# Kernel tuning notes

Hardware: AMD Instinct MI355X
Metric: run time of the kernel (lower is better)

Reference implementation:

```python
import jax, jax.numpy as jnp
import numpy as np
from jax import lax

B, T, C, DIN, DOUT = 32, 128, 64, 32, 32  # batch, output_channels(seq), input_channels, input_dim, output_dim


def _init_params(key):
    # Mirror torch init: xOps zeros with identity on min(dout,din) diag; hOps = eye.
    # Add small noise so gradients/behavior are non-degenerate.
    k1, k2 = jax.random.split(key)
    eye_x = jnp.zeros((DOUT, DIN), jnp.float32).at[jnp.arange(min(DOUT, DIN)), jnp.arange(min(DOUT, DIN))].set(1.0)
    xOps = jnp.broadcast_to(eye_x, (4, T, C, DOUT, DIN)) + 0.02 * jax.random.normal(k1, (4, T, C, DOUT, DIN), jnp.float32)
    hOps = jnp.broadcast_to(jnp.eye(DOUT, dtype=jnp.float32), (4, T, C, DOUT, DOUT)) + 0.02 * jax.random.normal(k2, (4, T, C, DOUT, DOUT), jnp.float32)
    return xOps, hOps


def setup_inputs() -> dict:
    key = jax.random.key(0)
    kx, kp = jax.random.split(key)
    x = jax.random.normal(kx, (B, T, C, DIN), jnp.float32)
    xOps, hOps = _init_params(kp)
    return {"x": x, "xOps": xOps, "hOps": hOps}


def reference(x, xOps, hOps):
    # x: [B,T,C,Din]; xOps: [4,T,C,Dout,Din]; hOps: [4,T,C,Dout,Dout]
    b, t, c, _ = x.shape
    dout = hOps.shape[-1]
    h0 = jnp.zeros((b, c, dout), x.dtype)
    c0 = jnp.zeros((b, c, dout), x.dtype)

    def step(carry, inp):
        h, cc = carry
        x_t, xop_t, hop_t = inp  # [B,C,Din], [4,C,Dout,Din], [4,C,Dout,Dout]
        # per-channel (grouped) gate pre-activations, 4 gates at once
        X = jnp.einsum('gcij,bcj->gbci', xop_t, x_t) + jnp.einsum('gcij,bcj->gbci', hop_t, h)
        i = jax.nn.sigmoid(X[0])
        f = jax.nn.sigmoid(X[1])
        g = jnp.tanh(X[2])
        o = jax.nn.sigmoid(X[3])
        c_new = f * cc + i * g
        h_new = o * jnp.tanh(c_new)
        return (h_new, c_new), None

    xs = (jnp.swapaxes(x, 0, 1), jnp.swapaxes(xOps, 0, 1), jnp.swapaxes(hOps, 0, 1))
    (h_fin, _), _ = lax.scan(step, (h0, c0), xs)
    return h_fin  # [B,C,Dout]
```

## Files before the change

### kernel.cpp

```cpp
#include <hip/hip_runtime.h>
#include <stdint.h>

#define T_STEPS 128
#define C_CH    64
#define D_IN    32
#define D_OUT   32

#define RS 72

using frag_ab = __attribute__((ext_vector_type(8))) short;
using frag_cd = __attribute__((ext_vector_type(4))) float;

__device__ __forceinline__ void lds_barrier() {
  asm volatile("s_waitcnt lgkmcnt(0)\n\ts_barrier" ::: "memory");
}

__device__ __forceinline__ uint32_t pack_hi16(uint32_t u0, uint32_t u1) {
  return __builtin_amdgcn_perm(u1, u0, 0x07060302u);
}

__device__ __forceinline__ float fast_sigmoid(float v) {
  return __builtin_amdgcn_rcpf(1.0f + __expf(-v));
}
__device__ __forceinline__ float fast_tanh(float v) {
  return fmaf(2.0f, __builtin_amdgcn_rcpf(1.0f + __expf(-2.0f * v)), -1.0f);
}

__global__ void __launch_bounds__(256)
lstm_kernel(const float* __restrict__ x, const float* __restrict__ xOps,
            const float* __restrict__ hOps, float* __restrict__ out) {
  __shared__ short Ahi[128 * RS];
  __shared__ short Alo[128 * RS];
  __shared__ short Bhi[16 * RS];
  __shared__ short Blo[16 * RS];
  __shared__ float exch[4 * 32 * 9];

  const int tid = threadIdx.x;
  const int c   = blockIdx.x & 63;
  const int q   = blockIdx.x >> 6;

  for (int idx = tid; idx < (16 * RS) / 2; idx += 256) {
    ((uint32_t*)Bhi)[idx] = 0u;
    ((uint32_t*)Blo)[idx] = 0u;
  }

  const float* wptr[8];
  int wlds[8];
#pragma unroll
  for (int it = 0; it < 8; ++it) {
    int f  = (it * 256 + tid) * 4;
    int fh = f & 4095;
    int g  = fh >> 10;
    int i  = (fh >> 5) & 31;
    int j  = fh & 31;
    const float* base = (f < 4096) ? xOps : hOps;
    wptr[it] = base + (size_t)g * (T_STEPS * C_CH * 1024) + (size_t)c * 1024 + i * 32 + j;
    int k = j + ((f < 4096) ? 0 : 32);
    wlds[it] = (g * 32 + i) * RS + k;
  }

  const float* xptr = x;
  int xlds = 0;
  if (tid < 128) {
    int bl = tid >> 4;
    int kp = (tid & 15) * 2;
    int bg = q * 8 + bl;
    xptr = x + (size_t)bg * (T_STEPS * C_CH * D_IN) + (size_t)c * D_IN + kp;
    xlds = bl * RS + kp;
  }

  const int wave   = tid >> 6;
  const int lane   = tid & 63;
  const int frag_n = lane & 15;
  const int quad   = lane >> 4;

  const int eb = tid >> 5;
  const int ei = tid & 31;

  float4 wv[8];
#pragma unroll
  for (int it = 0; it < 8; ++it) wv[it] = *(const float4*)wptr[it];
  float2 xv = make_float2(0.f, 0.f);
  if (tid < 128) xv = *(const float2*)xptr;

  lds_barrier();

  float c_state = 0.0f;

#pragma unroll 1
  for (int t = 0; t < T_STEPS; ++t) {
#pragma unroll
    for (int it = 0; it < 8; ++it) {
      float4 v = wv[it];
      uint32_t u0 = __float_as_uint(v.x), u1 = __float_as_uint(v.y);
      uint32_t u2 = __float_as_uint(v.z), u3 = __float_as_uint(v.w);
      float r0 = v.x - __uint_as_float(u0 & 0xFFFF0000u);
      float r1 = v.y - __uint_as_float(u1 & 0xFFFF0000u);
      float r2 = v.z - __uint_as_float(u2 & 0xFFFF0000u);
      float r3 = v.w - __uint_as_float(u3 & 0xFFFF0000u);
      int s = wlds[it];
      *(uint2*)&Ahi[s] = make_uint2(pack_hi16(u0, u1), pack_hi16(u2, u3));
      *(uint2*)&Alo[s] = make_uint2(pack_hi16(__float_as_uint(r0), __float_as_uint(r1)),
                                    pack_hi16(__float_as_uint(r2), __float_as_uint(r3)));
    }
    if (tid < 128) {
      uint32_t u0 = __float_as_uint(xv.x), u1 = __float_as_uint(xv.y);
      float r0 = xv.x - __uint_as_float(u0 & 0xFFFF0000u);
      float r1 = xv.y - __uint_as_float(u1 & 0xFFFF0000u);
      *(uint32_t*)&Bhi[xlds] = pack_hi16(u0, u1);
      *(uint32_t*)&Blo[xlds] = pack_hi16(__float_as_uint(r0), __float_as_uint(r1));
    }

    if (t + 1 < T_STEPS) {
#pragma unroll
      for (int it = 0; it < 8; ++it)
        wv[it] = *(const float4*)(wptr[it] + (size_t)(t + 1) * (C_CH * 1024));
      if (tid < 128) xv = *(const float2*)(xptr + (size_t)(t + 1) * (C_CH * D_IN));
    }

    lds_barrier();

    frag_cd acc0 = {0.f, 0.f, 0.f, 0.f};
    frag_cd acc1 = {0.f, 0.f, 0.f, 0.f};
#pragma unroll
    for (int kt = 0; kt < 2; ++kt) {
      const int kk = kt * 32 + quad * 8;
      frag_ab bh = *(const frag_ab*)&Bhi[frag_n * RS + kk];
      frag_ab bl = *(const frag_ab*)&Blo[frag_n * RS + kk];
      {
        int m = wave * 32 + frag_n;
        frag_ab ah = *(const frag_ab*)&Ahi[m * RS + kk];
        frag_ab al = *(const frag_ab*)&Alo[m * RS + kk];
        acc0 = __builtin_amdgcn_mfma_f32_16x16x32_bf16(ah, bh, acc0, 0, 0, 0);
        acc0 = __builtin_amdgcn_mfma_f32_16x16x32_bf16(ah, bl, acc0, 0, 0, 0);
        acc0 = __builtin_amdgcn_mfma_f32_16x16x32_bf16(al, bh, acc0, 0, 0, 0);
      }
      {
        int m = wave * 32 + 16 + frag_n;
        frag_ab ah = *(const frag_ab*)&Ahi[m * RS + kk];
        frag_ab al = *(const frag_ab*)&Alo[m * RS + kk];
        acc1 = __builtin_amdgcn_mfma_f32_16x16x32_bf16(ah, bh, acc1, 0, 0, 0);
        acc1 = __builtin_amdgcn_mfma_f32_16x16x32_bf16(ah, bl, acc1, 0, 0, 0);
        acc1 = __builtin_amdgcn_mfma_f32_16x16x32_bf16(al, bh, acc1, 0, 0, 0);
      }
    }

    if (frag_n < 8) {
#pragma unroll
      for (int r = 0; r < 4; ++r) {
        exch[(wave * 32 + quad * 4 + r) * 9 + frag_n]      = acc0[r];
        exch[(wave * 32 + 16 + quad * 4 + r) * 9 + frag_n] = acc1[r];
      }
    }

    lds_barrier();

    {
      float X0 = exch[(0 * 32 + ei) * 9 + eb];
      float X1 = exch[(1 * 32 + ei) * 9 + eb];
      float X2 = exch[(2 * 32 + ei) * 9 + eb];
      float X3 = exch[(3 * 32 + ei) * 9 + eb];
      float ig = fast_sigmoid(X0);
      float fg = fast_sigmoid(X1);
      float gg = fast_tanh(X2);
      float og = fast_sigmoid(X3);
      c_state = fg * c_state + ig * gg;
      float hval = og * fast_tanh(c_state);
      if (t == T_STEPS - 1) {
        out[((size_t)(q * 8 + eb) * C_CH + c) * D_OUT + ei] = hval;
      } else {
        uint32_t u  = __float_as_uint(hval);
        float    r  = hval - __uint_as_float(u & 0xFFFF0000u);
        uint32_t ru = __float_as_uint(r);
        uint32_t pu  = __shfl_xor(u, 1, 64);
        uint32_t pru = __shfl_xor(ru, 1, 64);
        if ((ei & 1) == 0) {
          *(uint32_t*)&Bhi[eb * RS + 32 + ei] = pack_hi16(u, pu);
          *(uint32_t*)&Blo[eb * RS + 32 + ei] = pack_hi16(ru, pru);
        }
      }
    }
  }
}

extern "C" void kernel_launch(void* const* d_in, const int* in_sizes, int n_in,
                              void* d_out, int out_size, void* d_ws, size_t ws_size,
                              hipStream_t stream) {
  const float* x    = (const float*)d_in[0];
  const float* xOps = (const float*)d_in[1];
  const float* hOps = (const float*)d_in[2];
  lstm_kernel<<<dim3(256), dim3(256), 0, stream>>>(x, xOps, hOps, (float*)d_out);
}
```

Measured before the change: 359.2 us.

## Stream weights via async global-to-LDS loads with double buffering and in-register gates

Weight tiles now go straight from global memory into double-buffered LDS through global_load_lds, and the bf16 hi/lo split is done in registers at MFMA operand load time rather than on a staging write. Rows are permuted so each lane's accumulator holds all four gates for one output element, which removes the exchange buffer and one barrier per step. The block grows to 512 threads (8 waves), each issuing a single MFMA chain, and the loop is unrolled by two. This trades more threads, XOR-swizzled LDS indexing and a vmcnt wait per step for a shorter serial critical path per timestep.

```diff
diff --git a/kernel.cpp b/kernel.cpp
--- a/kernel.cpp
+++ b/kernel.cpp
@@ -3,17 +3,10 @@
 
 #define T_STEPS 128
 #define C_CH    64
-#define D_IN    32
-#define D_OUT   32
-
-#define RS 72
 
 using frag_ab = __attribute__((ext_vector_type(8))) short;
 using frag_cd = __attribute__((ext_vector_type(4))) float;
-
-__device__ __forceinline__ void lds_barrier() {
-  asm volatile("s_waitcnt lgkmcnt(0)\n\ts_barrier" ::: "memory");
-}
+typedef __attribute__((ext_vector_type(4))) uint32_t u32x4;
 
 __device__ __forceinline__ uint32_t pack_hi16(uint32_t u0, uint32_t u1) {
   return __builtin_amdgcn_perm(u1, u0, 0x07060302u);
@@ -26,159 +19,161 @@
   return fmaf(2.0f, __builtin_amdgcn_rcpf(1.0f + __expf(-2.0f * v)), -1.0f);
 }
 
-__global__ void __launch_bounds__(256)
+__device__ __forceinline__ void async_load16(const float* g, void* l) {
+  __builtin_amdgcn_global_load_lds((const __attribute__((address_space(1))) void*)g,
+                                   (__attribute__((address_space(3))) void*)l, 16, 0, 0);
+}
+
+struct Frag2 { frag_ab hi, lo; };
+
+__device__ __forceinline__ Frag2 split8(float4 a, float4 b) {
+  uint32_t u0 = __float_as_uint(a.x), u1 = __float_as_uint(a.y);
+  uint32_t u2 = __float_as_uint(a.z), u3 = __float_as_uint(a.w);
+  uint32_t u4 = __float_as_uint(b.x), u5 = __float_as_uint(b.y);
+  uint32_t u6 = __float_as_uint(b.z), u7 = __float_as_uint(b.w);
+  uint32_t r0 = __float_as_uint(a.x - __uint_as_float(u0 & 0xFFFF0000u));
+  uint32_t r1 = __float_as_uint(a.y - __uint_as_float(u1 & 0xFFFF0000u));
+  uint32_t r2 = __float_as_uint(a.z - __uint_as_float(u2 & 0xFFFF0000u));
+  uint32_t r3 = __float_as_uint(a.w - __uint_as_float(u3 & 0xFFFF0000u));
+  uint32_t r4 = __float_as_uint(b.x - __uint_as_float(u4 & 0xFFFF0000u));
+  uint32_t r5 = __float_as_uint(b.y - __uint_as_float(u5 & 0xFFFF0000u));
+  uint32_t r6 = __float_as_uint(b.z - __uint_as_float(u6 & 0xFFFF0000u));
+  uint32_t r7 = __float_as_uint(b.w - __uint_as_float(u7 & 0xFFFF0000u));
+  union { u32x4 v; frag_ab f; } H, L;
+  H.v[0] = pack_hi16(u0, u1); H.v[1] = pack_hi16(u2, u3);
+  H.v[2] = pack_hi16(u4, u5); H.v[3] = pack_hi16(u6, u7);
+  L.v[0] = pack_hi16(r0, r1); L.v[1] = pack_hi16(r2, r3);
+  L.v[2] = pack_hi16(r4, r5); L.v[3] = pack_hi16(r6, r7);
+  Frag2 o; o.hi = H.f; o.lo = L.f; return o;
+}
+
+__global__ void __launch_bounds__(512)
 lstm_kernel(const float* __restrict__ x, const float* __restrict__ xOps,
             const float* __restrict__ hOps, float* __restrict__ out) {
-  __shared__ short Ahi[128 * RS];
-  __shared__ short Alo[128 * RS];
-  __shared__ short Bhi[16 * RS];
-  __shared__ short Blo[16 * RS];
-  __shared__ float exch[4 * 32 * 9];
+  __shared__ __align__(16) float Afp[2][2][128][32];
+  __shared__ __align__(16) short Bq[2][2][2][4][16][8];
 
-  const int tid = threadIdx.x;
-  const int c   = blockIdx.x & 63;
-  const int q   = blockIdx.x >> 6;
-
-  for (int idx = tid; idx < (16 * RS) / 2; idx += 256) {
-    ((uint32_t*)Bhi)[idx] = 0u;
-    ((uint32_t*)Blo)[idx] = 0u;
-  }
-
-  const float* wptr[8];
-  int wlds[8];
-#pragma unroll
-  for (int it = 0; it < 8; ++it) {
-    int f  = (it * 256 + tid) * 4;
-    int fh = f & 4095;
-    int g  = fh >> 10;
-    int i  = (fh >> 5) & 31;
-    int j  = fh & 31;
-    const float* base = (f < 4096) ? xOps : hOps;
-    wptr[it] = base + (size_t)g * (T_STEPS * C_CH * 1024) + (size_t)c * 1024 + i * 32 + j;
-    int k = j + ((f < 4096) ? 0 : 32);
-    wlds[it] = (g * 32 + i) * RS + k;
-  }
-
-  const float* xptr = x;
-  int xlds = 0;
-  if (tid < 128) {
-    int bl = tid >> 4;
-    int kp = (tid & 15) * 2;
-    int bg = q * 8 + bl;
-    xptr = x + (size_t)bg * (T_STEPS * C_CH * D_IN) + (size_t)c * D_IN + kp;
-    xlds = bl * RS + kp;
-  }
-
-  const int wave   = tid >> 6;
+  const int tid    = threadIdx.x;
+  const int c      = blockIdx.x & 63;
+  const int q      = blockIdx.x >> 6;
+  const int w      = tid >> 6;
   const int lane   = tid & 63;
   const int frag_n = lane & 15;
   const int quad   = lane >> 4;
 
-  const int eb = tid >> 5;
-  const int ei = tid & 31;
+  int apl[4], arb[4];
+  const float* aptr[4];
+#pragma unroll
+  for (int ii = 0; ii < 4; ++ii) {
+    const int idx = w + 8 * ii;
+    const int pl  = idx >> 4;
+    const int rb  = idx & 15;
+    apl[ii] = pl; arb[ii] = rb;
+    const int r    = rb * 8 + (lane >> 3);
+    const int g    = r >> 5;
+    const int i    = r & 31;
+    const int f    = ((r >> 5) << 1) | (r & 1);
+    const int slot = (lane & 7) ^ f;
+    const float* base = pl ? hOps : xOps;
+    aptr[ii] = base + ((size_t)g * T_STEPS * C_CH + c) * 1024
+                    + (size_t)i * 32 + slot * 4;
+  }
 
-  float4 wv[8];
+  const bool xthr = (tid < 128);
+  const int  xn   = (tid >> 4) & 7;
+  const int  xjp  = (tid & 15) * 2;
+  const float* xptr = x + (size_t)(q * 8 + xn) * (T_STEPS * C_CH * 32)
+                        + c * 32 + xjp;
+
+  for (int idx = tid; idx < 4096; idx += 512) ((uint32_t*)Bq)[idx] = 0u;
+  __syncthreads();
+
 #pragma unroll
-  for (int it = 0; it < 8; ++it) wv[it] = *(const float4*)wptr[it];
+  for (int ii = 0; ii < 4; ++ii) {
+    async_load16(aptr[ii], &Afp[0][apl[ii]][arb[ii] * 8][0]);
+    aptr[ii] += (size_t)C_CH * 1024;
+  }
   float2 xv = make_float2(0.f, 0.f);
-  if (tid < 128) xv = *(const float2*)xptr;
+  if (xthr) {
+    float2 x0 = *(const float2*)xptr;
+    uint32_t u0 = __float_as_uint(x0.x), u1 = __float_as_uint(x0.y);
+    float r0 = x0.x - __uint_as_float(u0 & 0xFFFF0000u);
+    float r1 = x0.y - __uint_as_float(u1 & 0xFFFF0000u);
+    const int kg = xjp >> 3, sl = xjp & 7;
+    *(uint32_t*)&Bq[0][0][0][kg][xn][sl] = pack_hi16(u0, u1);
+    *(uint32_t*)&Bq[0][0][1][kg][xn][sl] =
+        pack_hi16(__float_as_uint(r0), __float_as_uint(r1));
+    xv = *(const float2*)(xptr + (size_t)C_CH * 32);
+  }
+  asm volatile("s_waitcnt vmcnt(0) lgkmcnt(0)\n\ts_barrier" ::: "memory");
 
-  lds_barrier();
+  const int frow = (frag_n & 3) * 32 + 4 * w + (frag_n >> 2);
+  const int ff   = ((frow >> 5) << 1) | (frow & 1);
+  const int so0  = (((quad << 1) ^ ff) << 2);
+  const int so1  = ((((quad << 1) | 1) ^ ff) << 2);
+  const int iq   = 4 * w + quad;
+  const int hkg  = iq >> 3, hsl = iq & 7;
 
   float c_state = 0.0f;
 
-#pragma unroll 1
+#pragma unroll 2
   for (int t = 0; t < T_STEPS; ++t) {
-#pragma unroll
-    for (int it = 0; it < 8; ++it) {
-      float4 v = wv[it];
-      uint32_t u0 = __float_as_uint(v.x), u1 = __float_as_uint(v.y);
-      uint32_t u2 = __float_as_uint(v.z), u3 = __float_as_uint(v.w);
-      float r0 = v.x - __uint_as_float(u0 & 0xFFFF0000u);
-      float r1 = v.y - __uint_as_float(u1 & 0xFFFF0000u);
-      float r2 = v.z - __uint_as_float(u2 & 0xFFFF0000u);
-      float r3 = v.w - __uint_as_float(u3 & 0xFFFF0000u);
-      int s = wlds[it];
-      *(uint2*)&Ahi[s] = make_uint2(pack_hi16(u0, u1), pack_hi16(u2, u3));
-      *(uint2*)&Alo[s] = make_uint2(pack_hi16(__float_as_uint(r0), __float_as_uint(r1)),
-                                    pack_hi16(__float_as_uint(r2), __float_as_uint(r3)));
-    }
-    if (tid < 128) {
-      uint32_t u0 = __float_as_uint(xv.x), u1 = __float_as_uint(xv.y);
-      float r0 = xv.x - __uint_as_float(u0 & 0xFFFF0000u);
-      float r1 = xv.y - __uint_as_float(u1 & 0xFFFF0000u);
-      *(uint32_t*)&Bhi[xlds] = pack_hi16(u0, u1);
-      *(uint32_t*)&Blo[xlds] = pack_hi16(__float_as_uint(r0), __float_as_uint(r1));
-    }
+    const int cb = t & 1, nb = cb ^ 1;
 
     if (t + 1 < T_STEPS) {
 #pragma unroll
-      for (int it = 0; it < 8; ++it)
-        wv[it] = *(const float4*)(wptr[it] + (size_t)(t + 1) * (C_CH * 1024));
-      if (tid < 128) xv = *(const float2*)(xptr + (size_t)(t + 1) * (C_CH * D_IN));
-    }
-
-    lds_barrier();
-
-    frag_cd acc0 = {0.f, 0.f, 0.f, 0.f};
-    frag_cd acc1 = {0.f, 0.f, 0.f, 0.f};
-#pragma unroll
-    for (int kt = 0; kt < 2; ++kt) {
-      const int kk = kt * 32 + quad * 8;
-      frag_ab bh = *(const frag_ab*)&Bhi[frag_n * RS + kk];
-      frag_ab bl = *(const frag_ab*)&Blo[frag_n * RS + kk];
-      {
-        int m = wave * 32 + frag_n;
-        frag_ab ah = *(const frag_ab*)&Ahi[m * RS + kk];
-        frag_ab al = *(const frag_ab*)&Alo[m * RS + kk];
-        acc0 = __builtin_amdgcn_mfma_f32_16x16x32_bf16(ah, bh, acc0, 0, 0, 0);
-        acc0 = __builtin_amdgcn_mfma_f32_16x16x32_bf16(ah, bl, acc0, 0, 0, 0);
-        acc0 = __builtin_amdgcn_mfma_f32_16x16x32_bf16(al, bh, acc0, 0, 0, 0);
+      for (int ii = 0; ii < 4; ++ii) {
+        async_load16(aptr[ii], &Afp[nb][apl[ii]][arb[ii] * 8][0]);
+        aptr[ii] += (size_t)C_CH * 1024;
       }
-      {
-        int m = wave * 32 + 16 + frag_n;
-        frag_ab ah = *(const frag_ab*)&Ahi[m * RS + kk];
-        frag_ab al = *(const frag_ab*)&Alo[m * RS + kk];
-        acc1 = __builtin_amdgcn_mfma_f32_16x16x32_bf16(ah, bh, acc1, 0, 0, 0);
-        acc1 = __builtin_amdgcn_mfma_f32_16x16x32_bf16(ah, bl, acc1, 0, 0, 0);
-        acc1 = __builtin_amdgcn_mfma_f32_16x16x32_bf16(al, bh, acc1, 0, 0, 0);
+      if (xthr) {
+        uint32_t u0 = __float_as_uint(xv.x), u1 = __float_as_uint(xv.y);
+        float r0 = xv.x - __uint_as_float(u0 & 0xFFFF0000u);
+        float r1 = xv.y - __uint_as_float(u1 & 0xFFFF0000u);
+        const int kg = xjp >> 3, sl = xjp & 7;
+        *(uint32_t*)&Bq[nb][0][0][kg][xn][sl] = pack_hi16(u0, u1);
+        *(uint32_t*)&Bq[nb][0][1][kg][xn][sl] =
+            pack_hi16(__float_as_uint(r0), __float_as_uint(r1));
+        if (t + 2 < T_STEPS)
+          xv = *(const float2*)(xptr + (size_t)(t + 2) * (C_CH * 32));
       }
     }
 
-    if (frag_n < 8) {
+    frag_cd acc = {0.f, 0.f, 0.f, 0.f};
 #pragma unroll
-      for (int r = 0; r < 4; ++r) {
-        exch[(wave * 32 + quad * 4 + r) * 9 + frag_n]      = acc0[r];
-        exch[(wave * 32 + 16 + quad * 4 + r) * 9 + frag_n] = acc1[r];
-      }
+    for (int kt = 0; kt < 2; ++kt) {
+      const float* Ap = &Afp[cb][kt][frow][0];
+      const float4 va = *(const float4*)(Ap + so0);
+      const float4 vb = *(const float4*)(Ap + so1);
+      Frag2 A = split8(va, vb);
+      const frag_ab bh = *(const frag_ab*)&Bq[cb][kt][0][quad][frag_n][0];
+      const frag_ab bl = *(const frag_ab*)&Bq[cb][kt][1][quad][frag_n][0];
+      acc = __builtin_amdgcn_mfma_f32_16x16x32_bf16(A.hi, bh, acc, 0, 0, 0);
+      acc = __builtin_amdgcn_mfma_f32_16x16x32_bf16(A.hi, bl, acc, 0, 0, 0);
+      acc = __builtin_amdgcn_mfma_f32_16x16x32_bf16(A.lo, bh, acc, 0, 0, 0);
     }
 
-    lds_barrier();
+    const float ig = fast_sigmoid(acc[0]);
+    const float fg = fast_sigmoid(acc[1]);
+    const float gg = fast_tanh(acc[2]);
+    const float og = fast_sigmoid(acc[3]);
+    c_state = fg * c_state + ig * gg;
+    const float hval = og * fast_tanh(c_state);
 
-    {
-      float X0 = exch[(0 * 32 + ei) * 9 + eb];
-      float X1 = exch[(1 * 32 + ei) * 9 + eb];
-      float X2 = exch[(2 * 32 + ei) * 9 + eb];
-      float X3 = exch[(3 * 32 + ei) * 9 + eb];
-      float ig = fast_sigmoid(X0);
-      float fg = fast_sigmoid(X1);
-      float gg = fast_tanh(X2);
-      float og = fast_sigmoid(X3);
-      c_state = fg * c_state + ig * gg;
-      float hval = og * fast_tanh(c_state);
-      if (t == T_STEPS - 1) {
-        out[((size_t)(q * 8 + eb) * C_CH + c) * D_OUT + ei] = hval;
-      } else {
-        uint32_t u  = __float_as_uint(hval);
-        float    r  = hval - __uint_as_float(u & 0xFFFF0000u);
-        uint32_t ru = __float_as_uint(r);
-        uint32_t pu  = __shfl_xor(u, 1, 64);
-        uint32_t pru = __shfl_xor(ru, 1, 64);
-        if ((ei & 1) == 0) {
-          *(uint32_t*)&Bhi[eb * RS + 32 + ei] = pack_hi16(u, pu);
-          *(uint32_t*)&Blo[eb * RS + 32 + ei] = pack_hi16(ru, pru);
-        }
+    if (t == T_STEPS - 1) {
+      if (frag_n < 8)
+        out[((size_t)(q * 8 + frag_n) * C_CH + c) * 32 + iq] = hval;
+    } else {
+      uint32_t uh = __float_as_uint(hval);
+      float    rh = hval - __uint_as_float(uh & 0xFFFF0000u);
+      uint32_t ur = __float_as_uint(rh);
+      uint32_t pu = __shfl_xor(uh, 16);
+      uint32_t pr = __shfl_xor(ur, 16);
+      if (((quad & 1) == 0) && (frag_n < 8)) {
+        *(uint32_t*)&Bq[nb][1][0][hkg][frag_n][hsl] = pack_hi16(uh, pu);
+        *(uint32_t*)&Bq[nb][1][1][hkg][frag_n][hsl] = pack_hi16(ur, pr);
       }
+      asm volatile("s_waitcnt vmcnt(0) lgkmcnt(0)\n\ts_barrier" ::: "memory");
     }
   }
 }
@@ -189,5 +184,5 @@
   const float* x    = (const float*)d_in[0];
   const float* xOps = (const float*)d_in[1];
   const float* hOps = (const float*)d_in[2];
-  lstm_kernel<<<dim3(256), dim3(256), 0, stream>>>(x, xOps, hOps, (float*)d_out);
+  lstm_kernel<<<dim3(256), dim3(512), 0, stream>>>(x, xOps, hOps, (float*)d_out);
 }
```

Result: slower. 406.5 us (+13.2%).
